# Optimization experiments

Hardware: AMD Instinct MI355X
Metric: run time of the kernel (lower is better)

The kernel has to match this reference:

```python
import jax, jax.numpy as jnp
import numpy as np

N, K, C0, H = 256, 16, 16, 32  # vertices, regular degree, input feats, hidden


def setup_inputs() -> dict:
    key = jax.random.key(0)
    ks = jax.random.split(key, 4)
    # k-regular circulant graph: neighbors of i are i+/-1..i+/-K//2 (mod N), sorted by vertex id
    offs = np.concatenate([np.arange(1, K // 2 + 1), -np.arange(1, K // 2 + 1)])
    nbrs = np.sort((np.arange(N)[:, None] + offs[None, :]) % N, axis=1).astype(np.int32)
    X = jax.random.normal(ks[0], (N, C0), jnp.float32)
    W1 = jax.random.normal(ks[1], (18 * C0, H), jnp.float32) / np.sqrt(18 * C0)
    b1 = jnp.zeros((H,), jnp.float32)
    W2 = jax.random.normal(ks[2], (18 * H, H), jnp.float32) / np.sqrt(18 * H)
    b2 = jnp.zeros((H,), jnp.float32)
    fc_w = jax.random.normal(ks[3], (H, 1), jnp.float32) / np.sqrt(H)
    fc_b = jnp.zeros((1,), jnp.float32)
    return {"X": X, "nbrs": jnp.asarray(nbrs), "W1": W1, "b1": b1,
            "W2": W2, "b2": b2, "fc_w": fc_w, "fc_b": fc_b}


def contract18(T, A):
    """All 18 contractions of F6[t,a,b,e,f,c] = T[t,a,b,c] * A[e,f],
    exactly matching _collapse6to3 (_c6to2_111 + _c6to2_12 + _c6to2_3),
    without materializing the 6-d tensor.
    T: (n, k, k, k, c) with axes (vertex, t, a, b, channel); A: (k, k).
    Returns (n, k, k, 18*c)."""
    S = A.sum()            # total sum of A
    r = A.sum(1)           # row sums
    tr = jnp.trace(A)
    sum_b = T.sum(3)              # (n,t,a,c)
    sum_t = T.sum(1)              # (n,a,b,c)
    sum_ab = T.sum((2, 3))        # (n,t,c)
    sum_tb = T.sum((1, 3))        # (n,a,c)
    sum_all = T.sum((1, 2, 3))    # (n,c)
    # _c6to2_111 (5 permutations)
    c1 = sum_b * S
    c2 = sum_ab[:, :, None, :] * r[None, None, :, None]
    c3 = sum_t * S
    c4 = sum_tb[:, :, None, :] * r[None, None, :, None]
    c5 = sum_all[:, None, None, :] * A[None, :, :, None]
    # _c6to2_12 (1 nontrivial permutation + 9 identical identity permutations)
    c6 = jnp.einsum('ntabc,b->ntac', T, r)
    c7 = sum_b * tr  # repeated 9 times, as in the source
    # _c6to2_3 (3 planar-diagonal contractions)
    d_ab = jnp.diagonal(T, axis1=2, axis2=3).transpose(0, 1, 3, 2)   # (n,t,a,c): T[t,a,a,c]
    c16 = jnp.einsum('ntac,ea->ntec', d_ab, A)
    d_tb = jnp.diagonal(T, axis1=1, axis2=3)                          # (n,a,c,t): T[t,a,t,c]
    c17 = jnp.einsum('nact,et->naec', d_tb, A)
    d_ttt = jnp.einsum('ntttc->ntc', T).sum(1)                        # (n,c)
    c18 = d_ttt[:, None, None, :] * A[None, :, :, None]
    return jnp.concatenate([c1, c2, c3, c4, c5, c6] + [c7] * 9 + [c16, c17, c18], axis=-1)


def _forward(X, nbrs, W1, b1, W2, b2, fc_w, fc_b):
    n, k = nbrs.shape
    # chi_{i,t}[a,p] = 1 iff a-th neighbor of i == p-th neighbor of j, j = nbrs[i,t]
    NN = nbrs[nbrs]                                                    # (n,k,k)
    CH = (nbrs[:, None, :, None] == NN[:, :, None, :]).astype(X.dtype)  # (n,t,a,p)
    A = jnp.eye(k, dtype=X.dtype)  # chi_{i,i} is the k x k identity for every i

    # get_F0: broadcast vertex features to (n, k, k, c0)
    F = jnp.broadcast_to(X[:, None, None, :], (n, k, k, X.shape[1]))

    def layer(F, W, b):
        Fg = F[nbrs]                                             # (n,t,p,q,c) gather neighbor features
        tmp = jnp.einsum('ntap,ntpqc->ntaqc', CH, Fg)            # chi @ F
        T = jnp.einsum('ntaqc,ntbq->ntabc', tmp, CH)             # (chi @ F) @ chi^T
        col = contract18(T, A)                                   # (n,k,k,18c)
        return jax.nn.relu(col @ W + b)

    F1 = layer(F, W1, b1)
    F2 = layer(F1, W2, b2)
    # get_Troot then full sum: chi_root scatters F2 entries injectively into [n,n,c],
    # so sum over Troot == sum over all entries of F2.
    g = F2.sum((0, 1, 2))                                        # (H,)
    return g @ fc_w + fc_b                                       # (1,)


def reference(X, nbrs, W1, b1, W2, b2, fc_w, fc_b):
    return _forward(X, nbrs, W1, b1, W2, b2, fc_w, fc_b)
```

## Files before the change

### kernel.cpp

```cpp
#include <hip/hip_runtime.h>


constexpr int KN = 16, HH = 32, NV = 256, C2 = 32;

__device__ __forceinline__ float rlane(float v, int l) {
    return __int_as_float(__builtin_amdgcn_readlane(__float_as_int(v), l));
}

#define MM_RL(WPTR, NB, COEF_EXPR, ACC) do {                                   \
    _Pragma("unroll")                                                          \
    for (int B = 0; B < (NB); ++B) {                                           \
        const float4 w_ = ((const float4*)(WPTR))[B * 64 + lane];              \
        _Pragma("unroll")                                                      \
        for (int cc = 0; cc < 8; ++cc) {                                       \
            const int ci = B * 8 + cc;                                         \
            const float cf_ = (COEF_EXPR);                                     \
            _Pragma("unroll")                                                  \
            for (int h4 = 0; h4 < 8; ++h4) {                                   \
                const int src_ = 8 * cc + h4;                                  \
                (ACC)[4*h4+0] = fmaf(cf_, rlane(w_.x, src_), (ACC)[4*h4+0]);   \
                (ACC)[4*h4+1] = fmaf(cf_, rlane(w_.y, src_), (ACC)[4*h4+1]);   \
                (ACC)[4*h4+2] = fmaf(cf_, rlane(w_.z, src_), (ACC)[4*h4+2]);   \
                (ACC)[4*h4+3] = fmaf(cf_, rlane(w_.w, src_), (ACC)[4*h4+3]);   \
            }                                                                  \
        }                                                                      \
    }                                                                          \
} while (0)

__global__ __launch_bounds__(512)
void ccn_l1(const float* __restrict__ X, const int* __restrict__ nbrs,
            const float* __restrict__ W1, const float* __restrict__ bias,
            float* __restrict__ F1c, float* __restrict__ outz)
{
    __shared__ float sE1[6 * 512];
    __shared__ float sPP[256 * 36];
    __shared__ float sX[16][20];
    __shared__ float sV[16][164];
    __shared__ int   s_nbi[16];
    __shared__ int   s_nbj[16][17];
    __shared__ int   s_P[16][16];
    __shared__ int   s_vm[16];
    __shared__ float s_m[16];

    const int tid  = threadIdx.x;
    const int i    = ((blockIdx.x & 7) << 5) | (blockIdx.x >> 3);
    const int lane = tid & 63;

    if (blockIdx.x == 0 && tid == 0) outz[0] = 0.f;
    if (tid < 16) s_nbi[tid] = nbrs[i * 16 + tid];
    __syncthreads();

    if (tid < 256) {
        const int t = tid >> 4, y = tid & 15;
        const int j = s_nbi[t];
        s_nbj[t][y] = nbrs[j * 16 + y];
        sX[t][y]    = X[j * 16 + y];
    } else {
        const int u = tid - 256;
        float acc = 0.f;
        #pragma unroll
        for (int g = 6; g < 15; ++g) acc += W1[g * 512 + u];
        sE1[u]        = 16.f * W1[u] + W1[5 * 512 + u] + 16.f * acc;
        sE1[512 + u]  = W1[512 + u];
        sE1[1024 + u] = W1[15 * 512 + u];
        sE1[1536 + u] = 16.f * W1[2 * 512 + u];
        sE1[2048 + u] = W1[3 * 512 + u];
        sE1[2560 + u] = W1[4 * 512 + u];
    }
    __syncthreads();

    if (tid < 256) {
        const int t = tid >> 4, y = tid & 15;
        const int tgt = s_nbi[y];
        int p = -1;
        #pragma unroll
        for (int q = 0; q < 16; ++q) if (s_nbj[t][q] == tgt) p = q;
        s_P[t][y] = p;
        unsigned long long bal = __ballot(p >= 0);
        if (y == 0) {
            int vm = (int)((bal >> ((t & 3) * 16)) & 0xFFFFull);
            s_vm[t] = vm;
            s_m[t]  = (float)__popc(vm);
        }
    } else {
        const int u = tid;
        float acc = 0.f;
        #pragma unroll
        for (int g = 6; g < 15; ++g) acc += W1[g * 512 + u];
        sE1[u]        = 16.f * W1[u] + W1[5 * 512 + u] + 16.f * acc;
        sE1[512 + u]  = W1[512 + u];
        sE1[1024 + u] = W1[15 * 512 + u];
        sE1[1536 + u] = 16.f * W1[2 * 512 + u];
        sE1[2048 + u] = W1[3 * 512 + u];
        sE1[2560 + u] = W1[4 * 512 + u];
    }
    __syncthreads();

    if (tid < 256) {
        const int t = tid >> 4, y = tid & 15, x = t;
        float Y0[16];
        #pragma unroll
        for (int c4 = 0; c4 < 4; ++c4) {
            float4 v = *(const float4*)&sX[t][4 * c4];
            Y0[4*c4+0] = v.x; Y0[4*c4+1] = v.y; Y0[4*c4+2] = v.z; Y0[4*c4+3] = v.w;
        }
        float Z4[16], Z5[16];
        #pragma unroll
        for (int c = 0; c < 16; ++c) { Z4[c] = 0.f; Z5[c] = 0.f; }
        #pragma unroll
        for (int tp = 0; tp < 16; ++tp) {
            const int vm = s_vm[tp];
            const float mt = s_m[tp];
            const float fb = ((vm >> x) & 1) ? mt : 0.f;
            const float f5 = mt * mt;
            #pragma unroll
            for (int c4 = 0; c4 < 4; ++c4) {
                float4 v = *(const float4*)&sX[tp][4 * c4];
                Z4[4*c4+0] = fmaf(fb, v.x, Z4[4*c4+0]);
                Z4[4*c4+1] = fmaf(fb, v.y, Z4[4*c4+1]);
                Z4[4*c4+2] = fmaf(fb, v.z, Z4[4*c4+2]);
                Z4[4*c4+3] = fmaf(fb, v.w, Z4[4*c4+3]);
                Z5[4*c4+0] = fmaf(f5, v.x, Z5[4*c4+0]);
                Z5[4*c4+1] = fmaf(f5, v.y, Z5[4*c4+1]);
                Z5[4*c4+2] = fmaf(f5, v.z, Z5[4*c4+2]);
                Z5[4*c4+3] = fmaf(f5, v.w, Z5[4*c4+3]);
            }
        }
        const float m = s_m[t];
        float v0a=0.f,v0b=0.f,v1a=0.f,v1b=0.f,v2a=0.f,v2b=0.f;
        float v3a=0.f,v3b=0.f,v4a=0.f,v4b=0.f;
        const float2* Wsb = (const float2*)(sE1 + 0 * 512);
        const float2* Wab = (const float2*)(sE1 + 1 * 512);
        const float2* W16 = (const float2*)(sE1 + 2 * 512);
        const float2* Wtb = (const float2*)(sE1 + 4 * 512);
        const float2* Wal = (const float2*)(sE1 + 5 * 512);
        #pragma unroll
        for (int c = 0; c < 16; ++c) {
            const float cf0 = m * Y0[c];
            const float cf1 = m * cf0;
            const float cf2 = Y0[c];
            const float cf3 = Z4[c];
            const float cf4 = Z5[c];
            const int idx = c * 16 + y;
            float2 w0 = Wsb[idx]; v0a = fmaf(cf0, w0.x, v0a); v0b = fmaf(cf0, w0.y, v0b);
            float2 w1 = Wab[idx]; v1a = fmaf(cf1, w1.x, v1a); v1b = fmaf(cf1, w1.y, v1b);
            float2 w2 = W16[idx]; v2a = fmaf(cf2, w2.x, v2a); v2b = fmaf(cf2, w2.y, v2b);
            float2 w3 = Wtb[idx]; v3a = fmaf(cf3, w3.x, v3a); v3b = fmaf(cf3, w3.y, v3b);
            float2 w4 = Wal[idx]; v4a = fmaf(cf4, w4.x, v4a); v4b = fmaf(cf4, w4.y, v4b);
        }
        *(float2*)&sV[t][0 * 32 + 2 * y] = make_float2(v0a, v0b);
        *(float2*)&sV[t][1 * 32 + 2 * y] = make_float2(v1a, v1b);
        *(float2*)&sV[t][2 * 32 + 2 * y] = make_float2(v2a, v2b);
        *(float2*)&sV[t][3 * 32 + 2 * y] = make_float2(v3a, v3b);
        *(float2*)&sV[t][4 * 32 + 2 * y] = make_float2(v4a, v4b);
    } else {
        const int w = tid - 256;
        const int t = w >> 4, y = w & 15, x = t;
        float Z2[16];
        #pragma unroll
        for (int c = 0; c < 16; ++c) Z2[c] = 0.f;
        #pragma unroll
        for (int tp = 0; tp < 16; ++tp) {
            const int vm = s_vm[tp];
            const float f2 = (float)((vm >> x) & (vm >> y) & 1);
            #pragma unroll
            for (int c4 = 0; c4 < 4; ++c4) {
                float4 v = *(const float4*)&sX[tp][4 * c4];
                Z2[4*c4+0] = fmaf(f2, v.x, Z2[4*c4+0]);
                Z2[4*c4+1] = fmaf(f2, v.y, Z2[4*c4+1]);
                Z2[4*c4+2] = fmaf(f2, v.z, Z2[4*c4+2]);
                Z2[4*c4+3] = fmaf(f2, v.w, Z2[4*c4+3]);
            }
        }
        float pp[HH];
        #pragma unroll
        for (int h = 0; h < HH; ++h) pp[h] = 0.f;
        MM_RL(sE1 + 3 * 512, 2, Z2[ci], pp);
        float* dst = &sPP[(t * 16 + y) * 36];
        #pragma unroll
        for (int h4 = 0; h4 < 8; ++h4)
            *(float4*)&dst[4 * h4] = make_float4(pp[4*h4], pp[4*h4+1], pp[4*h4+2], pp[4*h4+3]);
    }
    __syncthreads();

    float fr[HH];
    if (tid < 256) {
        const int t = tid >> 4, y = tid & 15, x = t;
        const float vy  = (s_P[t][y] >= 0) ? 1.f : 0.f;
        const float dxy = (x == y) ? 1.f : 0.f;
        const float* pp = &sPP[(t * 16 + y) * 36];
        #pragma unroll
        for (int h4 = 0; h4 < 8; ++h4) {
            const float4 V0 = *(const float4*)&sV[t][0 * 32 + 4 * h4];
            const float4 V1 = *(const float4*)&sV[t][1 * 32 + 4 * h4];
            const float4 V2 = *(const float4*)&sV[t][2 * 32 + 4 * h4];
            const float4 V3 = *(const float4*)&sV[t][3 * 32 + 4 * h4];
            const float4 V4 = *(const float4*)&sV[t][4 * 32 + 4 * h4];
            const float4 PP = *(const float4*)&pp[4 * h4];
            float a_ = vy*(V0.x+V2.x) + V1.x + V3.x + dxy*V4.x + PP.x + bias[4*h4+0];
            float b_ = vy*(V0.y+V2.y) + V1.y + V3.y + dxy*V4.y + PP.y + bias[4*h4+1];
            float c_ = vy*(V0.z+V2.z) + V1.z + V3.z + dxy*V4.z + PP.z + bias[4*h4+2];
            float d_ = vy*(V0.w+V2.w) + V1.w + V3.w + dxy*V4.w + PP.w + bias[4*h4+3];
            fr[4*h4+0] = a_ > 0.f ? a_ : 0.f;
            fr[4*h4+1] = b_ > 0.f ? b_ : 0.f;
            fr[4*h4+2] = c_ > 0.f ? c_ : 0.f;
            fr[4*h4+3] = d_ > 0.f ? d_ : 0.f;
        }
    }
    __syncthreads();

    if (tid < 256) {
        const int t = tid >> 4, y = tid & 15;
        float* dst = &sPP[(y * 16 + t) * 36];
        #pragma unroll
        for (int h4 = 0; h4 < 8; ++h4)
            *(float4*)&dst[4 * h4] = make_float4(fr[4*h4], fr[4*h4+1], fr[4*h4+2], fr[4*h4+3]);
    }
    __syncthreads();

    if (tid < 256) {
        const int q = tid >> 4, p = tid & 15;
        const float* src = &sPP[(q * 16 + p) * 36];
        float4* F4 = (float4*)F1c;
        const size_t basec = ((size_t)i * 16 + q) * 128 + p;
        #pragma unroll
        for (int c4 = 0; c4 < 8; ++c4)
            F4[basec + c4 * 16] = *(const float4*)&src[4 * c4];
    }
}

__global__ __launch_bounds__(512)
void ccn_l2(const float* __restrict__ F1c, const int* __restrict__ nbrs,
            const float* __restrict__ W2, const float* __restrict__ bias,
            const float* __restrict__ fcw, const float* __restrict__ fcb,
            float* __restrict__ out)
{
    __shared__ float sE2[6 * 1024];
    __shared__ float sRpp[256 * 36];
    __shared__ float s_stb[16 * 33];
    __shared__ float s_sall[C2];
    __shared__ int   s_nbi[16];
    __shared__ int   s_PQ[16 * 17];
    __shared__ float s_red[4];

    const int tid  = threadIdx.x;
    const int i    = ((blockIdx.x & 7) << 5) | (blockIdx.x >> 3);
    const int lane = tid & 63;
    const float4* F4 = (const float4*)F1c;

    if (tid < 16) s_nbi[tid] = nbrs[i * 16 + tid];
    __syncthreads();

    if (tid < 256) {
        const int t = tid >> 4, y = tid & 15;
        const int j = s_nbi[t];
        s_PQ[t * 17 + y] = nbrs[j * 16 + y];
    } else {
        const int w = tid - 256;
        #pragma unroll
        for (int k = 0; k < 2; ++k) {
            const int u = w + k * 256;
            float acc = 0.f;
            #pragma unroll
            for (int g = 6; g < 15; ++g) acc += W2[g * 1024 + u];
            sE2[u]        = 16.f * W2[u] + W2[5 * 1024 + u] + 16.f * acc;
            sE2[1024 + u] = W2[1024 + u];
            sE2[2048 + u] = W2[15 * 1024 + u];
            sE2[3072 + u] = 16.f * W2[2 * 1024 + u];
            sE2[4096 + u] = W2[3 * 1024 + u];
            sE2[5120 + u] = W2[4 * 1024 + u];
        }
    }
    __syncthreads();

    if (tid < 256) {
        const int t = tid >> 4, y = tid & 15;
        const int tgt = s_nbi[y];
        int p = -1;
        #pragma unroll
        for (int q = 0; q < 16; ++q) if (s_PQ[t * 17 + q] == tgt) p = q;
        s_PQ[t * 17 + y] = p;
    } else {
        const int w = tid - 256;
        #pragma unroll
        for (int k = 2; k < 4; ++k) {
            const int u = w + k * 256;
            float acc = 0.f;
            #pragma unroll
            for (int g = 6; g < 15; ++g) acc += W2[g * 1024 + u];
            sE2[u]        = 16.f * W2[u] + W2[5 * 1024 + u] + 16.f * acc;
            sE2[1024 + u] = W2[1024 + u];
            sE2[2048 + u] = W2[15 * 1024 + u];
            sE2[3072 + u] = 16.f * W2[2 * 1024 + u];
            sE2[4096 + u] = W2[3 * 1024 + u];
            sE2[5120 + u] = W2[4 * 1024 + u];
        }
    }
    __syncthreads();

    float pre[HH];
    float sab[C2];
    float pp[HH];

    if (tid < 256) {
        const int t = tid >> 4, y = tid & 15;
        const int j = s_nbi[t];
        const int p = s_PQ[t * 17 + y];
        const float mp = (p >= 0) ? 1.f : 0.f;
        const int pc = p >= 0 ? p : 0;
        const size_t jbase = (size_t)j * 2048;

        float R[C2];
        #pragma unroll
        for (int c = 0; c < C2; ++c) R[c] = 0.f;
        #pragma unroll
        for (int b = 0; b < 16; ++b) {
            const int q = s_PQ[t * 17 + b];
            const float mm = (q >= 0) ? mp : 0.f;
            const int qc = q >= 0 ? q : 0;
            const size_t rb = jbase + (size_t)qc * 128 + pc;
            #pragma unroll
            for (int c4 = 0; c4 < 8; ++c4) {
                float4 v = F4[rb + c4 * 16];
                R[4*c4+0] = fmaf(mm, v.x, R[4*c4+0]);
                R[4*c4+1] = fmaf(mm, v.y, R[4*c4+1]);
                R[4*c4+2] = fmaf(mm, v.z, R[4*c4+2]);
                R[4*c4+3] = fmaf(mm, v.w, R[4*c4+3]);
            }
        }
        #pragma unroll
        for (int c4 = 0; c4 < 8; ++c4)
            *(float4*)&sRpp[(t * 16 + y) * 36 + 4 * c4] =
                make_float4(R[4*c4+0], R[4*c4+1], R[4*c4+2], R[4*c4+3]);

        #pragma unroll
        for (int h = 0; h < HH; ++h) pre[h] = 0.f;
        MM_RL(sE2 + 0 * 1024, 4, R[ci], pre);

        #pragma unroll
        for (int c = 0; c < C2; ++c) {
            float s = R[c];
            s += __shfl_xor(s, 1);
            s += __shfl_xor(s, 2);
            s += __shfl_xor(s, 4);
            s += __shfl_xor(s, 8);
            sab[c] = s;
        }

        float D[C2];
        {
            const size_t db = jbase + (size_t)pc * 128 + pc;
            #pragma unroll
            for (int c4 = 0; c4 < 8; ++c4) {
                float4 v = F4[db + c4 * 16];
                D[4*c4+0] = mp * v.x; D[4*c4+1] = mp * v.y;
                D[4*c4+2] = mp * v.z; D[4*c4+3] = mp * v.w;
            }
        }
        MM_RL(sE2 + 2 * 1024, 4, D[ci], pre);
    } else {
        const int w = tid - 256;
        const int g = w >> 4, l = w & 15;
        float ST[C2];
        #pragma unroll
        for (int c = 0; c < C2; ++c) ST[c] = 0.f;
        #pragma unroll
        for (int tp = 0; tp < 16; ++tp) {
            const int jt = s_nbi[tp];
            const int py = s_PQ[tp * 17 + g];
            const int px = s_PQ[tp * 17 + l];
            const float mm = (px >= 0 && py >= 0) ? 1.f : 0.f;
            const int pyc = py >= 0 ? py : 0;
            const int pxc = px >= 0 ? px : 0;
            const size_t rb = (size_t)jt * 2048 + (size_t)pyc * 128 + pxc;
            #pragma unroll
            for (int c4 = 0; c4 < 8; ++c4) {
                float4 v = F4[rb + c4 * 16];
                ST[4*c4+0] = fmaf(mm, v.x, ST[4*c4+0]);
                ST[4*c4+1] = fmaf(mm, v.y, ST[4*c4+1]);
                ST[4*c4+2] = fmaf(mm, v.z, ST[4*c4+2]);
                ST[4*c4+3] = fmaf(mm, v.w, ST[4*c4+3]);
            }
        }
        #pragma unroll
        for (int h = 0; h < HH; ++h) pp[h] = 0.f;
        MM_RL(sE2 + 3 * 1024, 4, ST[ci], pp);
    }
    __syncthreads();

    if (tid < 256) {
        #pragma unroll
        for (int k = 0; k < 2; ++k) {
            const int x2 = (tid >> 5) + 8 * k;
            const int c = tid & 31;
            float s = 0.f;
            #pragma unroll
            for (int tt = 0; tt < 16; ++tt) s += sRpp[(tt * 16 + x2) * 36 + c];
            s_stb[x2 * 33 + c] = s;
        }
    }
    __syncthreads();

    if (tid < 256) {
        if (tid < 32) {
            float s = 0.f;
            #pragma unroll
            for (int x2 = 0; x2 < 16; ++x2) s += s_stb[x2 * 33 + tid];
            s_sall[tid] = s;
        }
    } else {
        const int w = tid - 256;
        const int g = w >> 4, l = w & 15;
        float* dst = &sRpp[(l * 16 + g) * 36];
        #pragma unroll
        for (int h4 = 0; h4 < 8; ++h4)
            *(float4*)&dst[4 * h4] = make_float4(pp[4*h4], pp[4*h4+1], pp[4*h4+2], pp[4*h4+3]);
    }
    __syncthreads();

    if (tid < 256) {
        const int t = tid >> 4, y = tid & 15, x = t;
        const float dxy = (x == y) ? 1.f : 0.f;
        float S0 = 0.f, S1 = 0.f, L0 = 0.f, L1 = 0.f;
        {
            const float2* Wab = (const float2*)(sE2 + 1 * 1024);
            const float2* Wtb = (const float2*)(sE2 + 4 * 1024);
            const float2* Wal = (const float2*)(sE2 + 5 * 1024);
            #pragma unroll
            for (int c = 0; c < C2; ++c) {
                const float cfa = sab[c];
                const float cft = s_stb[t * 33 + c];
                const float cfl = s_sall[c];
                const int idx = c * 16 + y;
                float2 wa = Wab[idx]; S0 = fmaf(cfa, wa.x, S0); S1 = fmaf(cfa, wa.y, S1);
                float2 wt = Wtb[idx]; S0 = fmaf(cft, wt.x, S0); S1 = fmaf(cft, wt.y, S1);
                float2 wl = Wal[idx]; L0 = fmaf(cfl, wl.x, L0); L1 = fmaf(cfl, wl.y, L1);
            }
        }
        const int gbase = (t & 3) * 16;
        #pragma unroll
        for (int h = 0; h < HH; ++h) {
            const int src = gbase + (h >> 1);
            const float sv = (h & 1) ? S1 : S0;
            const float lv = (h & 1) ? L1 : L0;
            pre[h] += __shfl(sv, src, 64) + dxy * __shfl(lv, src, 64);
        }
        {
            const float* ppr = &sRpp[(t * 16 + y) * 36];
            #pragma unroll
            for (int h4 = 0; h4 < 8; ++h4) {
                const float4 v = *(const float4*)&ppr[4 * h4];
                pre[4*h4+0] += v.x; pre[4*h4+1] += v.y;
                pre[4*h4+2] += v.z; pre[4*h4+3] += v.w;
            }
        }
        float local = 0.f;
        #pragma unroll
        for (int h = 0; h < HH; ++h) {
            float v = pre[h] + bias[h];
            v = v > 0.f ? v : 0.f;
            local += v * fcw[h];
        }
        #pragma unroll
        for (int off = 32; off > 0; off >>= 1) local += __shfl_down(local, off, 64);
        if (lane == 0) s_red[tid >> 6] = local;
    }
    __syncthreads();
    if (tid == 0) {
        const float v = s_red[0] + s_red[1] + s_red[2] + s_red[3]
                      + fcb[0] * (1.f / 256.f);
        atomicAdd(out, v);
    }
}

extern "C" void kernel_launch(void* const* d_in, const int* in_sizes, int n_in,
                              void* d_out, int out_size, void* d_ws, size_t ws_size,
                              hipStream_t stream) {
    const float* X    = (const float*)d_in[0];
    const int*   nbrs = (const int*)  d_in[1];
    const float* W1   = (const float*)d_in[2];
    const float* b1   = (const float*)d_in[3];
    const float* W2   = (const float*)d_in[4];
    const float* b2   = (const float*)d_in[5];
    const float* fc_w = (const float*)d_in[6];
    const float* fc_b = (const float*)d_in[7];
    float* outp = (float*)d_out;

    float* F1c = (float*)d_ws;

    ccn_l1<<<NV, 512, 0, stream>>>(X, nbrs, W1, b1, F1c, outp);
    ccn_l2<<<NV, 512, 0, stream>>>(F1c, nbrs, W2, b2, fc_w, fc_b, outp);
}
```

Measured before the change: 107.7 us.

## Fuse both CCN layers into one cooperative kernel with grid sync

Merges the two layer kernels into a single cooperative launch. A grid-wide barrier now separates the layer-1 output write from the layer-2 gather, and the two phases share one shared-memory union. The aim is to remove the second kernel launch and the gap between launches. In exchange it pays the cost of a cooperative launch and a grid barrier, and it needs all 256 blocks to be co-resident.

```diff
diff --git a/kernel.cpp b/kernel.cpp
--- a/kernel.cpp
+++ b/kernel.cpp
@@ -1,7 +1,10 @@
 #include <hip/hip_runtime.h>
+#include <hip/hip_cooperative_groups.h>
 
 
 constexpr int KN = 16, HH = 32, NV = 256, C2 = 32;
+
+namespace cg = cooperative_groups;
 
 __device__ __forceinline__ float rlane(float v, int l) {
     return __int_as_float(__builtin_amdgcn_readlane(__float_as_int(v), l));
@@ -27,449 +30,455 @@
     }                                                                          \
 } while (0)
 
+struct Phase1 {
+    float sE1[6 * 512];
+    float sPP[256 * 36];
+    float sX[16][20];
+    float sV[16][164];
+    int   s_nbi[16];
+    int   s_nbj[16][17];
+    int   s_P[16][16];
+    int   s_vm[16];
+    float s_m[16];
+};
+struct Phase2 {
+    float sE2[6 * 1024];
+    float sRpp[256 * 36];
+    float s_stb[16 * 33];
+    float s_sall[C2];
+    int   s_nbi[16];
+    int   s_PQ[16 * 17];
+    float s_red[4];
+};
+union SMem { Phase1 p1; Phase2 p2; };
+
 __global__ __launch_bounds__(512)
-void ccn_l1(const float* __restrict__ X, const int* __restrict__ nbrs,
-            const float* __restrict__ W1, const float* __restrict__ bias,
-            float* __restrict__ F1c, float* __restrict__ outz)
+void ccn_fused(const float* __restrict__ X, const int* __restrict__ nbrs,
+               const float* __restrict__ W1, const float* __restrict__ b1,
+               const float* __restrict__ W2, const float* __restrict__ b2,
+               const float* __restrict__ fcw, const float* __restrict__ fcb,
+               float* __restrict__ F1c, float* __restrict__ out)
 {
-    __shared__ float sE1[6 * 512];
-    __shared__ float sPP[256 * 36];
-    __shared__ float sX[16][20];
-    __shared__ float sV[16][164];
-    __shared__ int   s_nbi[16];
-    __shared__ int   s_nbj[16][17];
-    __shared__ int   s_P[16][16];
-    __shared__ int   s_vm[16];
-    __shared__ float s_m[16];
+    __shared__ __align__(16) SMem sm;
 
     const int tid  = threadIdx.x;
     const int i    = ((blockIdx.x & 7) << 5) | (blockIdx.x >> 3);
     const int lane = tid & 63;
 
-    if (blockIdx.x == 0 && tid == 0) outz[0] = 0.f;
-    if (tid < 16) s_nbi[tid] = nbrs[i * 16 + tid];
-    __syncthreads();
-
-    if (tid < 256) {
-        const int t = tid >> 4, y = tid & 15;
-        const int j = s_nbi[t];
-        s_nbj[t][y] = nbrs[j * 16 + y];
-        sX[t][y]    = X[j * 16 + y];
-    } else {
-        const int u = tid - 256;
-        float acc = 0.f;
-        #pragma unroll
-        for (int g = 6; g < 15; ++g) acc += W1[g * 512 + u];
-        sE1[u]        = 16.f * W1[u] + W1[5 * 512 + u] + 16.f * acc;
-        sE1[512 + u]  = W1[512 + u];
-        sE1[1024 + u] = W1[15 * 512 + u];
-        sE1[1536 + u] = 16.f * W1[2 * 512 + u];
-        sE1[2048 + u] = W1[3 * 512 + u];
-        sE1[2560 + u] = W1[4 * 512 + u];
+    {
+        Phase1& P = sm.p1;
+        if (blockIdx.x == 0 && tid == 0) out[0] = 0.f;
+        if (tid < 16) P.s_nbi[tid] = nbrs[i * 16 + tid];
+        __syncthreads();
+
+        if (tid < 256) {
+            const int t = tid >> 4, y = tid & 15;
+            const int j = P.s_nbi[t];
+            P.s_nbj[t][y] = nbrs[j * 16 + y];
+            P.sX[t][y]    = X[j * 16 + y];
+        } else {
+            const int u = tid - 256;
+            float acc = 0.f;
+            #pragma unroll
+            for (int g = 6; g < 15; ++g) acc += W1[g * 512 + u];
+            P.sE1[u]        = 16.f * W1[u] + W1[5 * 512 + u] + 16.f * acc;
+            P.sE1[512 + u]  = W1[512 + u];
+            P.sE1[1024 + u] = W1[15 * 512 + u];
+            P.sE1[1536 + u] = 16.f * W1[2 * 512 + u];
+            P.sE1[2048 + u] = W1[3 * 512 + u];
+            P.sE1[2560 + u] = W1[4 * 512 + u];
+        }
+        __syncthreads();
+
+        if (tid < 256) {
+            const int t = tid >> 4, y = tid & 15;
+            const int tgt = P.s_nbi[y];
+            int p = -1;
+            #pragma unroll
+            for (int q = 0; q < 16; ++q) if (P.s_nbj[t][q] == tgt) p = q;
+            P.s_P[t][y] = p;
+            unsigned long long bal = __ballot(p >= 0);
+            if (y == 0) {
+                int vm = (int)((bal >> ((t & 3) * 16)) & 0xFFFFull);
+                P.s_vm[t] = vm;
+                P.s_m[t]  = (float)__popc(vm);
+            }
+        } else {
+            const int u = tid;
+            float acc = 0.f;
+            #pragma unroll
+            for (int g = 6; g < 15; ++g) acc += W1[g * 512 + u];
+            P.sE1[u]        = 16.f * W1[u] + W1[5 * 512 + u] + 16.f * acc;
+            P.sE1[512 + u]  = W1[512 + u];
+            P.sE1[1024 + u] = W1[15 * 512 + u];
+            P.sE1[1536 + u] = 16.f * W1[2 * 512 + u];
+            P.sE1[2048 + u] = W1[3 * 512 + u];
+            P.sE1[2560 + u] = W1[4 * 512 + u];
+        }
+        __syncthreads();
+
+        if (tid < 256) {
+            const int t = tid >> 4, y = tid & 15, x = t;
+            float Y0[16];
+            #pragma unroll
+            for (int c4 = 0; c4 < 4; ++c4) {
+                float4 v = *(const float4*)&P.sX[t][4 * c4];
+                Y0[4*c4+0] = v.x; Y0[4*c4+1] = v.y; Y0[4*c4+2] = v.z; Y0[4*c4+3] = v.w;
+            }
+            float Z4[16], Z5[16];
+            #pragma unroll
+            for (int c = 0; c < 16; ++c) { Z4[c] = 0.f; Z5[c] = 0.f; }
+            #pragma unroll
+            for (int tp = 0; tp < 16; ++tp) {
+                const int vm = P.s_vm[tp];
+                const float mt = P.s_m[tp];
+                const float fb = ((vm >> x) & 1) ? mt : 0.f;
+                const float f5 = mt * mt;
+                #pragma unroll
+                for (int c4 = 0; c4 < 4; ++c4) {
+                    float4 v = *(const float4*)&P.sX[tp][4 * c4];
+                    Z4[4*c4+0] = fmaf(fb, v.x, Z4[4*c4+0]);
+                    Z4[4*c4+1] = fmaf(fb, v.y, Z4[4*c4+1]);
+                    Z4[4*c4+2] = fmaf(fb, v.z, Z4[4*c4+2]);
+                    Z4[4*c4+3] = fmaf(fb, v.w, Z4[4*c4+3]);
+                    Z5[4*c4+0] = fmaf(f5, v.x, Z5[4*c4+0]);
+                    Z5[4*c4+1] = fmaf(f5, v.y, Z5[4*c4+1]);
+                    Z5[4*c4+2] = fmaf(f5, v.z, Z5[4*c4+2]);
+                    Z5[4*c4+3] = fmaf(f5, v.w, Z5[4*c4+3]);
+                }
+            }
+            const float m = P.s_m[t];
+            float v0a=0.f,v0b=0.f,v1a=0.f,v1b=0.f,v2a=0.f,v2b=0.f;
+            float v3a=0.f,v3b=0.f,v4a=0.f,v4b=0.f;
+            const float2* Wsb = (const float2*)(P.sE1 + 0 * 512);
+            const float2* Wab = (const float2*)(P.sE1 + 1 * 512);
+            const float2* W16 = (const float2*)(P.sE1 + 2 * 512);
+            const float2* Wtb = (const float2*)(P.sE1 + 4 * 512);
+            const float2* Wal = (const float2*)(P.sE1 + 5 * 512);
+            #pragma unroll
+            for (int c = 0; c < 16; ++c) {
+                const float cf0 = m * Y0[c];
+                const float cf1 = m * cf0;
+                const float cf2 = Y0[c];
+                const float cf3 = Z4[c];
+                const float cf4 = Z5[c];
+                const int idx = c * 16 + y;
+                float2 w0 = Wsb[idx]; v0a = fmaf(cf0, w0.x, v0a); v0b = fmaf(cf0, w0.y, v0b);
+                float2 w1 = Wab[idx]; v1a = fmaf(cf1, w1.x, v1a); v1b = fmaf(cf1, w1.y, v1b);
+                float2 w2 = W16[idx]; v2a = fmaf(cf2, w2.x, v2a); v2b = fmaf(cf2, w2.y, v2b);
+                float2 w3 = Wtb[idx]; v3a = fmaf(cf3, w3.x, v3a); v3b = fmaf(cf3, w3.y, v3b);
+                float2 w4 = Wal[idx]; v4a = fmaf(cf4, w4.x, v4a); v4b = fmaf(cf4, w4.y, v4b);
+            }
+            *(float2*)&P.sV[t][0 * 32 + 2 * y] = make_float2(v0a, v0b);
+            *(float2*)&P.sV[t][1 * 32 + 2 * y] = make_float2(v1a, v1b);
+            *(float2*)&P.sV[t][2 * 32 + 2 * y] = make_float2(v2a, v2b);
+            *(float2*)&P.sV[t][3 * 32 + 2 * y] = make_float2(v3a, v3b);
+            *(float2*)&P.sV[t][4 * 32 + 2 * y] = make_float2(v4a, v4b);
+        } else {
+            const int w = tid - 256;
+            const int t = w >> 4, y = w & 15, x = t;
+            float Z2[16];
+            #pragma unroll
+            for (int c = 0; c < 16; ++c) Z2[c] = 0.f;
+            #pragma unroll
+            for (int tp = 0; tp < 16; ++tp) {
+                const int vm = P.s_vm[tp];
+                const float f2 = (float)((vm >> x) & (vm >> y) & 1);
+                #pragma unroll
+                for (int c4 = 0; c4 < 4; ++c4) {
+                    float4 v = *(const float4*)&P.sX[tp][4 * c4];
+                    Z2[4*c4+0] = fmaf(f2, v.x, Z2[4*c4+0]);
+                    Z2[4*c4+1] = fmaf(f2, v.y, Z2[4*c4+1]);
+                    Z2[4*c4+2] = fmaf(f2, v.z, Z2[4*c4+2]);
+                    Z2[4*c4+3] = fmaf(f2, v.w, Z2[4*c4+3]);
+                }
+            }
+            float pp[HH];
+            #pragma unroll
+            for (int h = 0; h < HH; ++h) pp[h] = 0.f;
+            MM_RL(P.sE1 + 3 * 512, 2, Z2[ci], pp);
+            float* dst = &P.sPP[(t * 16 + y) * 36];
+            #pragma unroll
+            for (int h4 = 0; h4 < 8; ++h4)
+                *(float4*)&dst[4 * h4] = make_float4(pp[4*h4], pp[4*h4+1], pp[4*h4+2], pp[4*h4+3]);
+        }
+        __syncthreads();
+
+        float fr[HH];
+        if (tid < 256) {
+            const int t = tid >> 4, y = tid & 15, x = t;
+            const float vy  = (P.s_P[t][y] >= 0) ? 1.f : 0.f;
+            const float dxy = (x == y) ? 1.f : 0.f;
+            const float* pp = &P.sPP[(t * 16 + y) * 36];
+            #pragma unroll
+            for (int h4 = 0; h4 < 8; ++h4) {
+                const float4 V0 = *(const float4*)&P.sV[t][0 * 32 + 4 * h4];
+                const float4 V1 = *(const float4*)&P.sV[t][1 * 32 + 4 * h4];
+                const float4 V2 = *(const float4*)&P.sV[t][2 * 32 + 4 * h4];
+                const float4 V3 = *(const float4*)&P.sV[t][3 * 32 + 4 * h4];
+                const float4 V4 = *(const float4*)&P.sV[t][4 * 32 + 4 * h4];
+                const float4 PP = *(const float4*)&pp[4 * h4];
+                float a_ = vy*(V0.x+V2.x) + V1.x + V3.x + dxy*V4.x + PP.x + b1[4*h4+0];
+                float b_ = vy*(V0.y+V2.y) + V1.y + V3.y + dxy*V4.y + PP.y + b1[4*h4+1];
+                float c_ = vy*(V0.z+V2.z) + V1.z + V3.z + dxy*V4.z + PP.z + b1[4*h4+2];
+                float d_ = vy*(V0.w+V2.w) + V1.w + V3.w + dxy*V4.w + PP.w + b1[4*h4+3];
+                fr[4*h4+0] = a_ > 0.f ? a_ : 0.f;
+                fr[4*h4+1] = b_ > 0.f ? b_ : 0.f;
+                fr[4*h4+2] = c_ > 0.f ? c_ : 0.f;
+                fr[4*h4+3] = d_ > 0.f ? d_ : 0.f;
+            }
+        }
+        __syncthreads();
+
+        if (tid < 256) {
+            const int t = tid >> 4, y = tid & 15;
+            float* dst = &P.sPP[(y * 16 + t) * 36];
+            #pragma unroll
+            for (int h4 = 0; h4 < 8; ++h4)
+                *(float4*)&dst[4 * h4] = make_float4(fr[4*h4], fr[4*h4+1], fr[4*h4+2], fr[4*h4+3]);
+        }
+        __syncthreads();
+
+        if (tid < 256) {
+            const int q = tid >> 4, p = tid & 15;
+            const float* src = &P.sPP[(q * 16 + p) * 36];
+            float4* F4 = (float4*)F1c;
+            const size_t basec = ((size_t)i * 16 + q) * 128 + p;
+            #pragma unroll
+            for (int c4 = 0; c4 < 8; ++c4)
+                F4[basec + c4 * 16] = *(const float4*)&src[4 * c4];
+        }
     }
-    __syncthreads();
-
-    if (tid < 256) {
-        const int t = tid >> 4, y = tid & 15;
-        const int tgt = s_nbi[y];
-        int p = -1;
-        #pragma unroll
-        for (int q = 0; q < 16; ++q) if (s_nbj[t][q] == tgt) p = q;
-        s_P[t][y] = p;
-        unsigned long long bal = __ballot(p >= 0);
-        if (y == 0) {
-            int vm = (int)((bal >> ((t & 3) * 16)) & 0xFFFFull);
-            s_vm[t] = vm;
-            s_m[t]  = (float)__popc(vm);
-        }
-    } else {
-        const int u = tid;
-        float acc = 0.f;
-        #pragma unroll
-        for (int g = 6; g < 15; ++g) acc += W1[g * 512 + u];
-        sE1[u]        = 16.f * W1[u] + W1[5 * 512 + u] + 16.f * acc;
-        sE1[512 + u]  = W1[512 + u];
-        sE1[1024 + u] = W1[15 * 512 + u];
-        sE1[1536 + u] = 16.f * W1[2 * 512 + u];
-        sE1[2048 + u] = W1[3 * 512 + u];
-        sE1[2560 + u] = W1[4 * 512 + u];
-    }
-    __syncthreads();
-
-    if (tid < 256) {
-        const int t = tid >> 4, y = tid & 15, x = t;
-        float Y0[16];
-        #pragma unroll
-        for (int c4 = 0; c4 < 4; ++c4) {
-            float4 v = *(const float4*)&sX[t][4 * c4];
-            Y0[4*c4+0] = v.x; Y0[4*c4+1] = v.y; Y0[4*c4+2] = v.z; Y0[4*c4+3] = v.w;
-        }
-        float Z4[16], Z5[16];
-        #pragma unroll
-        for (int c = 0; c < 16; ++c) { Z4[c] = 0.f; Z5[c] = 0.f; }
-        #pragma unroll
-        for (int tp = 0; tp < 16; ++tp) {
-            const int vm = s_vm[tp];
-            const float mt = s_m[tp];
-            const float fb = ((vm >> x) & 1) ? mt : 0.f;
-            const float f5 = mt * mt;
-            #pragma unroll
-            for (int c4 = 0; c4 < 4; ++c4) {
-                float4 v = *(const float4*)&sX[tp][4 * c4];
-                Z4[4*c4+0] = fmaf(fb, v.x, Z4[4*c4+0]);
-                Z4[4*c4+1] = fmaf(fb, v.y, Z4[4*c4+1]);
-                Z4[4*c4+2] = fmaf(fb, v.z, Z4[4*c4+2]);
-                Z4[4*c4+3] = fmaf(fb, v.w, Z4[4*c4+3]);
-                Z5[4*c4+0] = fmaf(f5, v.x, Z5[4*c4+0]);
-                Z5[4*c4+1] = fmaf(f5, v.y, Z5[4*c4+1]);
-                Z5[4*c4+2] = fmaf(f5, v.z, Z5[4*c4+2]);
-                Z5[4*c4+3] = fmaf(f5, v.w, Z5[4*c4+3]);
-            }
-        }
-        const float m = s_m[t];
-        float v0a=0.f,v0b=0.f,v1a=0.f,v1b=0.f,v2a=0.f,v2b=0.f;
-        float v3a=0.f,v3b=0.f,v4a=0.f,v4b=0.f;
-        const float2* Wsb = (const float2*)(sE1 + 0 * 512);
-        const float2* Wab = (const float2*)(sE1 + 1 * 512);
-        const float2* W16 = (const float2*)(sE1 + 2 * 512);
-        const float2* Wtb = (const float2*)(sE1 + 4 * 512);
-        const float2* Wal = (const float2*)(sE1 + 5 * 512);
-        #pragma unroll
-        for (int c = 0; c < 16; ++c) {
-            const float cf0 = m * Y0[c];
-            const float cf1 = m * cf0;
-            const float cf2 = Y0[c];
-            const float cf3 = Z4[c];
-            const float cf4 = Z5[c];
-            const int idx = c * 16 + y;
-            float2 w0 = Wsb[idx]; v0a = fmaf(cf0, w0.x, v0a); v0b = fmaf(cf0, w0.y, v0b);
-            float2 w1 = Wab[idx]; v1a = fmaf(cf1, w1.x, v1a); v1b = fmaf(cf1, w1.y, v1b);
-            float2 w2 = W16[idx]; v2a = fmaf(cf2, w2.x, v2a); v2b = fmaf(cf2, w2.y, v2b);
-            float2 w3 = Wtb[idx]; v3a = fmaf(cf3, w3.x, v3a); v3b = fmaf(cf3, w3.y, v3b);
-            float2 w4 = Wal[idx]; v4a = fmaf(cf4, w4.x, v4a); v4b = fmaf(cf4, w4.y, v4b);
-        }
-        *(float2*)&sV[t][0 * 32 + 2 * y] = make_float2(v0a, v0b);
-        *(float2*)&sV[t][1 * 32 + 2 * y] = make_float2(v1a, v1b);
-        *(float2*)&sV[t][2 * 32 + 2 * y] = make_float2(v2a, v2b);
-        *(float2*)&sV[t][3 * 32 + 2 * y] = make_float2(v3a, v3b);
-        *(float2*)&sV[t][4 * 32 + 2 * y] = make_float2(v4a, v4b);
-    } else {
-        const int w = tid - 256;
-        const int t = w >> 4, y = w & 15, x = t;
-        float Z2[16];
-        #pragma unroll
-        for (int c = 0; c < 16; ++c) Z2[c] = 0.f;
-        #pragma unroll
-        for (int tp = 0; tp < 16; ++tp) {
-            const int vm = s_vm[tp];
-            const float f2 = (float)((vm >> x) & (vm >> y) & 1);
-            #pragma unroll
-            for (int c4 = 0; c4 < 4; ++c4) {
-                float4 v = *(const float4*)&sX[tp][4 * c4];
-                Z2[4*c4+0] = fmaf(f2, v.x, Z2[4*c4+0]);
-                Z2[4*c4+1] = fmaf(f2, v.y, Z2[4*c4+1]);
-                Z2[4*c4+2] = fmaf(f2, v.z, Z2[4*c4+2]);
-                Z2[4*c4+3] = fmaf(f2, v.w, Z2[4*c4+3]);
-            }
-        }
+
+    cg::this_grid().sync();
+
+    {
+        Phase2& P = sm.p2;
+        const float4* F4 = (const float4*)F1c;
+
+        if (tid < 16) P.s_nbi[tid] = nbrs[i * 16 + tid];
+        __syncthreads();
+
+        if (tid < 256) {
+            const int t = tid >> 4, y = tid & 15;
+            const int j = P.s_nbi[t];
+            P.s_PQ[t * 17 + y] = nbrs[j * 16 + y];
+        } else {
+            const int w = tid - 256;
+            #pragma unroll
+            for (int k = 0; k < 2; ++k) {
+                const int u = w + k * 256;
+                float acc = 0.f;
+                #pragma unroll
+                for (int g = 6; g < 15; ++g) acc += W2[g * 1024 + u];
+                P.sE2[u]        = 16.f * W2[u] + W2[5 * 1024 + u] + 16.f * acc;
+                P.sE2[1024 + u] = W2[1024 + u];
+                P.sE2[2048 + u] = W2[15 * 1024 + u];
+                P.sE2[3072 + u] = 16.f * W2[2 * 1024 + u];
+                P.sE2[4096 + u] = W2[3 * 1024 + u];
+                P.sE2[5120 + u] = W2[4 * 1024 + u];
+            }
+        }
+        __syncthreads();
+
+        if (tid < 256) {
+            const int t = tid >> 4, y = tid & 15;
+            const int tgt = P.s_nbi[y];
+            int p = -1;
+            #pragma unroll
+            for (int q = 0; q < 16; ++q) if (P.s_PQ[t * 17 + q] == tgt) p = q;
+            P.s_PQ[t * 17 + y] = p;
+        } else {
+            const int w = tid - 256;
+            #pragma unroll
+            for (int k = 2; k < 4; ++k) {
+                const int u = w + k * 256;
+                float acc = 0.f;
+                #pragma unroll
+                for (int g = 6; g < 15; ++g) acc += W2[g * 1024 + u];
+                P.sE2[u]        = 16.f * W2[u] + W2[5 * 1024 + u] + 16.f * acc;
+                P.sE2[1024 + u] = W2[1024 + u];
+                P.sE2[2048 + u] = W2[15 * 1024 + u];
+                P.sE2[3072 + u] = 16.f * W2[2 * 1024 + u];
+                P.sE2[4096 + u] = W2[3 * 1024 + u];
+                P.sE2[5120 + u] = W2[4 * 1024 + u];
+            }
+        }
+        __syncthreads();
+
+        float pre[HH];
+        float sab[C2];
         float pp[HH];
-        #pragma unroll
-        for (int h = 0; h < HH; ++h) pp[h] = 0.f;
-        MM_RL(sE1 + 3 * 512, 2, Z2[ci], pp);
-        float* dst = &sPP[(t * 16 + y) * 36];
-        #pragma unroll
-        for (int h4 = 0; h4 < 8; ++h4)
-            *(float4*)&dst[4 * h4] = make_float4(pp[4*h4], pp[4*h4+1], pp[4*h4+2], pp[4*h4+3]);
-    }
-    __syncthreads();
-
-    float fr[HH];
-    if (tid < 256) {
-        const int t = tid >> 4, y = tid & 15, x = t;
-        const float vy  = (s_P[t][y] >= 0) ? 1.f : 0.f;
-        const float dxy = (x == y) ? 1.f : 0.f;
-        const float* pp = &sPP[(t * 16 + y) * 36];
-        #pragma unroll
-        for (int h4 = 0; h4 < 8; ++h4) {
-            const float4 V0 = *(const float4*)&sV[t][0 * 32 + 4 * h4];
-            const float4 V1 = *(const float4*)&sV[t][1 * 32 + 4 * h4];
-            const float4 V2 = *(const float4*)&sV[t][2 * 32 + 4 * h4];
-            const float4 V3 = *(const float4*)&sV[t][3 * 32 + 4 * h4];
-            const float4 V4 = *(const float4*)&sV[t][4 * 32 + 4 * h4];
-            const float4 PP = *(const float4*)&pp[4 * h4];
-            float a_ = vy*(V0.x+V2.x) + V1.x + V3.x + dxy*V4.x + PP.x + bias[4*h4+0];
-            float b_ = vy*(V0.y+V2.y) + V1.y + V3.y + dxy*V4.y + PP.y + bias[4*h4+1];
-            float c_ = vy*(V0.z+V2.z) + V1.z + V3.z + dxy*V4.z + PP.z + bias[4*h4+2];
-            float d_ = vy*(V0.w+V2.w) + V1.w + V3.w + dxy*V4.w + PP.w + bias[4*h4+3];
-            fr[4*h4+0] = a_ > 0.f ? a_ : 0.f;
-            fr[4*h4+1] = b_ > 0.f ? b_ : 0.f;
-            fr[4*h4+2] = c_ > 0.f ? c_ : 0.f;
-            fr[4*h4+3] = d_ > 0.f ? d_ : 0.f;
-        }
-    }
-    __syncthreads();
-
-    if (tid < 256) {
-        const int t = tid >> 4, y = tid & 15;
-        float* dst = &sPP[(y * 16 + t) * 36];
-        #pragma unroll
-        for (int h4 = 0; h4 < 8; ++h4)
-            *(float4*)&dst[4 * h4] = make_float4(fr[4*h4], fr[4*h4+1], fr[4*h4+2], fr[4*h4+3]);
-    }
-    __syncthreads();
-
-    if (tid < 256) {
-        const int q = tid >> 4, p = tid & 15;
-        const float* src = &sPP[(q * 16 + p) * 36];
-        float4* F4 = (float4*)F1c;
-        const size_t basec = ((size_t)i * 16 + q) * 128 + p;
-        #pragma unroll
-        for (int c4 = 0; c4 < 8; ++c4)
-            F4[basec + c4 * 16] = *(const float4*)&src[4 * c4];
-    }
-}
-
-__global__ __launch_bounds__(512)
-void ccn_l2(const float* __restrict__ F1c, const int* __restrict__ nbrs,
-            const float* __restrict__ W2, const float* __restrict__ bias,
-            const float* __restrict__ fcw, const float* __restrict__ fcb,
-            float* __restrict__ out)
-{
-    __shared__ float sE2[6 * 1024];
-    __shared__ float sRpp[256 * 36];
-    __shared__ float s_stb[16 * 33];
-    __shared__ float s_sall[C2];
-    __shared__ int   s_nbi[16];
-    __shared__ int   s_PQ[16 * 17];
-    __shared__ float s_red[4];
-
-    const int tid  = threadIdx.x;
-    const int i    = ((blockIdx.x & 7) << 5) | (blockIdx.x >> 3);
-    const int lane = tid & 63;
-    const float4* F4 = (const float4*)F1c;
-
-    if (tid < 16) s_nbi[tid] = nbrs[i * 16 + tid];
-    __syncthreads();
-
-    if (tid < 256) {
-        const int t = tid >> 4, y = tid & 15;
-        const int j = s_nbi[t];
-        s_PQ[t * 17 + y] = nbrs[j * 16 + y];
-    } else {
-        const int w = tid - 256;
-        #pragma unroll
-        for (int k = 0; k < 2; ++k) {
-            const int u = w + k * 256;
-            float acc = 0.f;
-            #pragma unroll
-            for (int g = 6; g < 15; ++g) acc += W2[g * 1024 + u];
-            sE2[u]        = 16.f * W2[u] + W2[5 * 1024 + u] + 16.f * acc;
-            sE2[1024 + u] = W2[1024 + u];
-            sE2[2048 + u] = W2[15 * 1024 + u];
-            sE2[3072 + u] = 16.f * W2[2 * 1024 + u];
-            sE2[4096 + u] = W2[3 * 1024 + u];
-            sE2[5120 + u] = W2[4 * 1024 + u];
-        }
-    }
-    __syncthreads();
-
-    if (tid < 256) {
-        const int t = tid >> 4, y = tid & 15;
-        const int tgt = s_nbi[y];
-        int p = -1;
-        #pragma unroll
-        for (int q = 0; q < 16; ++q) if (s_PQ[t * 17 + q] == tgt) p = q;
-        s_PQ[t * 17 + y] = p;
-    } else {
-        const int w = tid - 256;
-        #pragma unroll
-        for (int k = 2; k < 4; ++k) {
-            const int u = w + k * 256;
-            float acc = 0.f;
-            #pragma unroll
-            for (int g = 6; g < 15; ++g) acc += W2[g * 1024 + u];
-            sE2[u]        = 16.f * W2[u] + W2[5 * 1024 + u] + 16.f * acc;
-            sE2[1024 + u] = W2[1024 + u];
-            sE2[2048 + u] = W2[15 * 1024 + u];
-            sE2[3072 + u] = 16.f * W2[2 * 1024 + u];
-            sE2[4096 + u] = W2[3 * 1024 + u];
-            sE2[5120 + u] = W2[4 * 1024 + u];
-        }
-    }
-    __syncthreads();
-
-    float pre[HH];
-    float sab[C2];
-    float pp[HH];
-
-    if (tid < 256) {
-        const int t = tid >> 4, y = tid & 15;
-        const int j = s_nbi[t];
-        const int p = s_PQ[t * 17 + y];
-        const float mp = (p >= 0) ? 1.f : 0.f;
-        const int pc = p >= 0 ? p : 0;
-        const size_t jbase = (size_t)j * 2048;
-
-        float R[C2];
-        #pragma unroll
-        for (int c = 0; c < C2; ++c) R[c] = 0.f;
-        #pragma unroll
-        for (int b = 0; b < 16; ++b) {
-            const int q = s_PQ[t * 17 + b];
-            const float mm = (q >= 0) ? mp : 0.f;
-            const int qc = q >= 0 ? q : 0;
-            const size_t rb = jbase + (size_t)qc * 128 + pc;
-            #pragma unroll
-            for (int c4 = 0; c4 < 8; ++c4) {
-                float4 v = F4[rb + c4 * 16];
-                R[4*c4+0] = fmaf(mm, v.x, R[4*c4+0]);
-                R[4*c4+1] = fmaf(mm, v.y, R[4*c4+1]);
-                R[4*c4+2] = fmaf(mm, v.z, R[4*c4+2]);
-                R[4*c4+3] = fmaf(mm, v.w, R[4*c4+3]);
-            }
-        }
-        #pragma unroll
-        for (int c4 = 0; c4 < 8; ++c4)
-            *(float4*)&sRpp[(t * 16 + y) * 36 + 4 * c4] =
-                make_float4(R[4*c4+0], R[4*c4+1], R[4*c4+2], R[4*c4+3]);
-
-        #pragma unroll
-        for (int h = 0; h < HH; ++h) pre[h] = 0.f;
-        MM_RL(sE2 + 0 * 1024, 4, R[ci], pre);
-
-        #pragma unroll
-        for (int c = 0; c < C2; ++c) {
-            float s = R[c];
-            s += __shfl_xor(s, 1);
-            s += __shfl_xor(s, 2);
-            s += __shfl_xor(s, 4);
-            s += __shfl_xor(s, 8);
-            sab[c] = s;
-        }
-
-        float D[C2];
-        {
-            const size_t db = jbase + (size_t)pc * 128 + pc;
-            #pragma unroll
-            for (int c4 = 0; c4 < 8; ++c4) {
-                float4 v = F4[db + c4 * 16];
-                D[4*c4+0] = mp * v.x; D[4*c4+1] = mp * v.y;
-                D[4*c4+2] = mp * v.z; D[4*c4+3] = mp * v.w;
-            }
-        }
-        MM_RL(sE2 + 2 * 1024, 4, D[ci], pre);
-    } else {
-        const int w = tid - 256;
-        const int g = w >> 4, l = w & 15;
-        float ST[C2];
-        #pragma unroll
-        for (int c = 0; c < C2; ++c) ST[c] = 0.f;
-        #pragma unroll
-        for (int tp = 0; tp < 16; ++tp) {
-            const int jt = s_nbi[tp];
-            const int py = s_PQ[tp * 17 + g];
-            const int px = s_PQ[tp * 17 + l];
-            const float mm = (px >= 0 && py >= 0) ? 1.f : 0.f;
-            const int pyc = py >= 0 ? py : 0;
-            const int pxc = px >= 0 ? px : 0;
-            const size_t rb = (size_t)jt * 2048 + (size_t)pyc * 128 + pxc;
-            #pragma unroll
-            for (int c4 = 0; c4 < 8; ++c4) {
-                float4 v = F4[rb + c4 * 16];
-                ST[4*c4+0] = fmaf(mm, v.x, ST[4*c4+0]);
-                ST[4*c4+1] = fmaf(mm, v.y, ST[4*c4+1]);
-                ST[4*c4+2] = fmaf(mm, v.z, ST[4*c4+2]);
-                ST[4*c4+3] = fmaf(mm, v.w, ST[4*c4+3]);
-            }
-        }
-        #pragma unroll
-        for (int h = 0; h < HH; ++h) pp[h] = 0.f;
-        MM_RL(sE2 + 3 * 1024, 4, ST[ci], pp);
-    }
-    __syncthreads();
-
-    if (tid < 256) {
-        #pragma unroll
-        for (int k = 0; k < 2; ++k) {
-            const int x2 = (tid >> 5) + 8 * k;
-            const int c = tid & 31;
-            float s = 0.f;
-            #pragma unroll
-            for (int tt = 0; tt < 16; ++tt) s += sRpp[(tt * 16 + x2) * 36 + c];
-            s_stb[x2 * 33 + c] = s;
-        }
-    }
-    __syncthreads();
-
-    if (tid < 256) {
-        if (tid < 32) {
-            float s = 0.f;
-            #pragma unroll
-            for (int x2 = 0; x2 < 16; ++x2) s += s_stb[x2 * 33 + tid];
-            s_sall[tid] = s;
-        }
-    } else {
-        const int w = tid - 256;
-        const int g = w >> 4, l = w & 15;
-        float* dst = &sRpp[(l * 16 + g) * 36];
-        #pragma unroll
-        for (int h4 = 0; h4 < 8; ++h4)
-            *(float4*)&dst[4 * h4] = make_float4(pp[4*h4], pp[4*h4+1], pp[4*h4+2], pp[4*h4+3]);
-    }
-    __syncthreads();
-
-    if (tid < 256) {
-        const int t = tid >> 4, y = tid & 15, x = t;
-        const float dxy = (x == y) ? 1.f : 0.f;
-        float S0 = 0.f, S1 = 0.f, L0 = 0.f, L1 = 0.f;
-        {
-            const float2* Wab = (const float2*)(sE2 + 1 * 1024);
-            const float2* Wtb = (const float2*)(sE2 + 4 * 1024);
-            const float2* Wal = (const float2*)(sE2 + 5 * 1024);
+
+        if (tid < 256) {
+            const int t = tid >> 4, y = tid & 15;
+            const int j = P.s_nbi[t];
+            const int p = P.s_PQ[t * 17 + y];
+            const float mp = (p >= 0) ? 1.f : 0.f;
+            const int pc = p >= 0 ? p : 0;
+            const size_t jbase = (size_t)j * 2048;
+
+            float R[C2];
+            #pragma unroll
+            for (int c = 0; c < C2; ++c) R[c] = 0.f;
+            #pragma unroll
+            for (int b = 0; b < 16; ++b) {
+                const int q = P.s_PQ[t * 17 + b];
+                const float mm = (q >= 0) ? mp : 0.f;
+                const int qc = q >= 0 ? q : 0;
+                const size_t rb = jbase + (size_t)qc * 128 + pc;
+                #pragma unroll
+                for (int c4 = 0; c4 < 8; ++c4) {
+                    float4 v = F4[rb + c4 * 16];
+                    R[4*c4+0] = fmaf(mm, v.x, R[4*c4+0]);
+                    R[4*c4+1] = fmaf(mm, v.y, R[4*c4+1]);
+                    R[4*c4+2] = fmaf(mm, v.z, R[4*c4+2]);
+                    R[4*c4+3] = fmaf(mm, v.w, R[4*c4+3]);
+                }
+            }
+            #pragma unroll
+            for (int c4 = 0; c4 < 8; ++c4)
+                *(float4*)&P.sRpp[(t * 16 + y) * 36 + 4 * c4] =
+                    make_float4(R[4*c4+0], R[4*c4+1], R[4*c4+2], R[4*c4+3]);
+
+            #pragma unroll
+            for (int h = 0; h < HH; ++h) pre[h] = 0.f;
+            MM_RL(P.sE2 + 0 * 1024, 4, R[ci], pre);
+
             #pragma unroll
             for (int c = 0; c < C2; ++c) {
-                const float cfa = sab[c];
-                const float cft = s_stb[t * 33 + c];
-                const float cfl = s_sall[c];
-                const int idx = c * 16 + y;
-                float2 wa = Wab[idx]; S0 = fmaf(cfa, wa.x, S0); S1 = fmaf(cfa, wa.y, S1);
-                float2 wt = Wtb[idx]; S0 = fmaf(cft, wt.x, S0); S1 = fmaf(cft, wt.y, S1);
-                float2 wl = Wal[idx]; L0 = fmaf(cfl, wl.x, L0); L1 = fmaf(cfl, wl.y, L1);
-            }
-        }
-        const int gbase = (t & 3) * 16;
-        #pragma unroll
-        for (int h = 0; h < HH; ++h) {
-            const int src = gbase + (h >> 1);
-            const float sv = (h & 1) ? S1 : S0;
-            const float lv = (h & 1) ? L1 : L0;
-            pre[h] += __shfl(sv, src, 64) + dxy * __shfl(lv, src, 64);
-        }
-        {
-            const float* ppr = &sRpp[(t * 16 + y) * 36];
-            #pragma unroll
-            for (int h4 = 0; h4 < 8; ++h4) {
-                const float4 v = *(const float4*)&ppr[4 * h4];
-                pre[4*h4+0] += v.x; pre[4*h4+1] += v.y;
-                pre[4*h4+2] += v.z; pre[4*h4+3] += v.w;
-            }
-        }
-        float local = 0.f;
-        #pragma unroll
-        for (int h = 0; h < HH; ++h) {
-            float v = pre[h] + bias[h];
-            v = v > 0.f ? v : 0.f;
-            local += v * fcw[h];
-        }
-        #pragma unroll
-        for (int off = 32; off > 0; off >>= 1) local += __shfl_down(local, off, 64);
-        if (lane == 0) s_red[tid >> 6] = local;
-    }
-    __syncthreads();
-    if (tid == 0) {
-        const float v = s_red[0] + s_red[1] + s_red[2] + s_red[3]
-                      + fcb[0] * (1.f / 256.f);
-        atomicAdd(out, v);
+                float s = R[c];
+                s += __shfl_xor(s, 1);
+                s += __shfl_xor(s, 2);
+                s += __shfl_xor(s, 4);
+                s += __shfl_xor(s, 8);
+                sab[c] = s;
+            }
+
+            float D[C2];
+            {
+                const size_t db = jbase + (size_t)pc * 128 + pc;
+                #pragma unroll
+                for (int c4 = 0; c4 < 8; ++c4) {
+                    float4 v = F4[db + c4 * 16];
+                    D[4*c4+0] = mp * v.x; D[4*c4+1] = mp * v.y;
+                    D[4*c4+2] = mp * v.z; D[4*c4+3] = mp * v.w;
+                }
+            }
+            MM_RL(P.sE2 + 2 * 1024, 4, D[ci], pre);
+        } else {
+            const int w = tid - 256;
+            const int g = w >> 4, l = w & 15;
+            float ST[C2];
+            #pragma unroll
+            for (int c = 0; c < C2; ++c) ST[c] = 0.f;
+            #pragma unroll
+            for (int tp = 0; tp < 16; ++tp) {
+                const int jt = P.s_nbi[tp];
+                const int py = P.s_PQ[tp * 17 + g];
+                const int px = P.s_PQ[tp * 17 + l];
+                const float mm = (px >= 0 && py >= 0) ? 1.f : 0.f;
+                const int pyc = py >= 0 ? py : 0;
+                const int pxc = px >= 0 ? px : 0;
+                const size_t rb = (size_t)jt * 2048 + (size_t)pyc * 128 + pxc;
+                #pragma unroll
+                for (int c4 = 0; c4 < 8; ++c4) {
+                    float4 v = F4[rb + c4 * 16];
+                    ST[4*c4+0] = fmaf(mm, v.x, ST[4*c4+0]);
+                    ST[4*c4+1] = fmaf(mm, v.y, ST[4*c4+1]);
+                    ST[4*c4+2] = fmaf(mm, v.z, ST[4*c4+2]);
+                    ST[4*c4+3] = fmaf(mm, v.w, ST[4*c4+3]);
+                }
+            }
+            #pragma unroll
+            for (int h = 0; h < HH; ++h) pp[h] = 0.f;
+            MM_RL(P.sE2 + 3 * 1024, 4, ST[ci], pp);
+        }
+        __syncthreads();
+
+        if (tid < 256) {
+            #pragma unroll
+            for (int k = 0; k < 2; ++k) {
+                const int x2 = (tid >> 5) + 8 * k;
+                const int c = tid & 31;
+                float s = 0.f;
+                #pragma unroll
+                for (int tt = 0; tt < 16; ++tt) s += P.sRpp[(tt * 16 + x2) * 36 + c];
+                P.s_stb[x2 * 33 + c] = s;
+            }
+        }
+        __syncthreads();
+
+        if (tid < 256) {
+            if (tid < 32) {
+                float s = 0.f;
+                #pragma unroll
+                for (int x2 = 0; x2 < 16; ++x2) s += P.s_stb[x2 * 33 + tid];
+                P.s_sall[tid] = s;
+            }
+        } else {
+            const int w = tid - 256;
+            const int g = w >> 4, l = w & 15;
+            float* dst = &P.sRpp[(l * 16 + g) * 36];
+            #pragma unroll
+            for (int h4 = 0; h4 < 8; ++h4)
+                *(float4*)&dst[4 * h4] = make_float4(pp[4*h4], pp[4*h4+1], pp[4*h4+2], pp[4*h4+3]);
+        }
+        __syncthreads();
+
+        if (tid < 256) {
+            const int t = tid >> 4, y = tid & 15, x = t;
+            const float dxy = (x == y) ? 1.f : 0.f;
+            float S0 = 0.f, S1 = 0.f, L0 = 0.f, L1 = 0.f;
+            {
+                const float2* Wab = (const float2*)(P.sE2 + 1 * 1024);
+                const float2* Wtb = (const float2*)(P.sE2 + 4 * 1024);
+                const float2* Wal = (const float2*)(P.sE2 + 5 * 1024);
+                #pragma unroll
+                for (int c = 0; c < C2; ++c) {
+                    const float cfa = sab[c];
+                    const float cft = P.s_stb[t * 33 + c];
+                    const float cfl = P.s_sall[c];
+                    const int idx = c * 16 + y;
+                    float2 wa = Wab[idx]; S0 = fmaf(cfa, wa.x, S0); S1 = fmaf(cfa, wa.y, S1);
+                    float2 wt = Wtb[idx]; S0 = fmaf(cft, wt.x, S0); S1 = fmaf(cft, wt.y, S1);
+                    float2 wl = Wal[idx]; L0 = fmaf(cfl, wl.x, L0); L1 = fmaf(cfl, wl.y, L1);
+                }
+            }
+            const int gbase = (t & 3) * 16;
+            #pragma unroll
+            for (int h = 0; h < HH; ++h) {
+                const int src = gbase + (h >> 1);
+                const float sv = (h & 1) ? S1 : S0;
+                const float lv = (h & 1) ? L1 : L0;
+                pre[h] += __shfl(sv, src, 64) + dxy * __shfl(lv, src, 64);
+            }
+            {
+                const float* ppr = &P.sRpp[(t * 16 + y) * 36];
+                #pragma unroll
+                for (int h4 = 0; h4 < 8; ++h4) {
+                    const float4 v = *(const float4*)&ppr[4 * h4];
+                    pre[4*h4+0] += v.x; pre[4*h4+1] += v.y;
+                    pre[4*h4+2] += v.z; pre[4*h4+3] += v.w;
+                }
+            }
+            float local = 0.f;
+            #pragma unroll
+            for (int h = 0; h < HH; ++h) {
+                float v = pre[h] + b2[h];
+                v = v > 0.f ? v : 0.f;
+                local += v * fcw[h];
+            }
+            #pragma unroll
+            for (int off = 32; off > 0; off >>= 1) local += __shfl_down(local, off, 64);
+            if (lane == 0) P.s_red[tid >> 6] = local;
+        }
+        __syncthreads();
+        if (tid == 0) {
+            const float v = P.s_red[0] + P.s_red[1] + P.s_red[2] + P.s_red[3]
+                          + fcb[0] * (1.f / 256.f);
+            atomicAdd(out, v);
+        }
     }
 }
 
@@ -485,9 +494,11 @@
     const float* fc_w = (const float*)d_in[6];
     const float* fc_b = (const float*)d_in[7];
     float* outp = (float*)d_out;
-
-    float* F1c = (float*)d_ws;
-
-    ccn_l1<<<NV, 512, 0, stream>>>(X, nbrs, W1, b1, F1c, outp);
-    ccn_l2<<<NV, 512, 0, stream>>>(F1c, nbrs, W2, b2, fc_w, fc_b, outp);
+    float* F1c  = (float*)d_ws;
+
+    void* kargs[] = { (void*)&X, (void*)&nbrs, (void*)&W1, (void*)&b1,
+                      (void*)&W2, (void*)&b2, (void*)&fc_w, (void*)&fc_b,
+                      (void*)&F1c, (void*)&outp };
+    hipLaunchCooperativeKernel((void*)ccn_fused, dim3(NV), dim3(512),
+                               kargs, 0, stream);
 }
```

Measured after the change: 154.5 us. +43.4%, slower.
